# Performance work log

Measured on AMD Instinct MI355X. Metric: run time of the kernel, lower is better.

Reference implementation:

```python
import jax, jax.numpy as jnp
import numpy as np

INPUT, HIDDEN, OUTPUT = 512, 512, 512
B, S = 32, 2048


def setup_inputs() -> dict:
    key = jax.random.key(0)
    ks = jax.random.split(key, 8)
    s_in = 1.0 / np.sqrt(INPUT)
    s_h = 1.0 / np.sqrt(HIDDEN)
    return {
        "x": jax.random.normal(ks[0], (B, S, INPUT), dtype=jnp.float32),
        "W_xh": jax.random.uniform(ks[1], (HIDDEN, INPUT), jnp.float32, -s_in, s_in),
        "b_xh": jax.random.uniform(ks[2], (HIDDEN,), jnp.float32, -s_in, s_in),
        "W_hh": jax.random.uniform(ks[3], (HIDDEN, HIDDEN), jnp.float32, -s_h, s_h),
        "b_hh": jax.random.uniform(ks[4], (HIDDEN,), jnp.float32, -s_h, s_h),
        "b_h": jnp.zeros((HIDDEN,), jnp.float32),
        "W_fc": jax.random.uniform(ks[5], (OUTPUT, HIDDEN), jnp.float32, -s_h, s_h),
        "b_fc": jax.random.uniform(ks[6], (OUTPUT,), jnp.float32, -s_h, s_h),
    }


def reference(x, W_xh, b_xh, W_hh, b_hh, b_h, W_fc, b_fc):
    # Precompute the input projection for all timesteps in one big GEMM:
    # [B,S,I] @ [I,H] -> [B,S,H]; bias terms folded in once.
    xproj = jnp.einsum("bsi,hi->bsh", x, W_xh) + (b_xh + b_hh + b_h)
    h0 = jnp.zeros((x.shape[0], W_hh.shape[0]), x.dtype)

    def step(h, xp_t):
        h = jnp.tanh(xp_t + h @ W_hh.T)
        return h, None

    # scan over time: xproj transposed to [S,B,H]
    h_final, _ = jax.lax.scan(step, h0, jnp.swapaxes(xproj, 0, 1))
    return h_final @ W_fc.T + b_fc
```

## Files before the change

kernel.cpp:

```cpp
#include <hip/hip_runtime.h>

typedef _Float16 f16;
typedef _Float16 f16x8 __attribute__((ext_vector_type(8)));
typedef float    f32x4 __attribute__((ext_vector_type(4)));

#define NSTEP 2048
#define HID   512
#define BATCH 32
#define SEQL  2048

#define P1_AS 40

__global__ __launch_bounds__(256, 2) void xproj_kernel(
    const float* __restrict__ x, const float* __restrict__ Wxh,
    const float* __restrict__ bxh, const float* __restrict__ bhh,
    const float* __restrict__ bh, f16* __restrict__ xp)
{
    __shared__ __align__(16) f16 As[64 * P1_AS];
    __shared__ __align__(16) f16 Bs[512 * P1_AS];

    const int t = threadIdx.x;
    const int wave = t >> 6, lane = t & 63;
    const size_t mbase = (size_t)blockIdx.x * 64;

    f32x4 acc[4][8];
#pragma unroll
    for (int i = 0; i < 4; i++)
#pragma unroll
        for (int j = 0; j < 8; j++) acc[i][j] = (f32x4){0.f, 0.f, 0.f, 0.f};

    const int r_st = t >> 2;
    const int koff = (t & 3) * 8;

    for (int k0 = 0; k0 < 512; k0 += 32) {
        __syncthreads();
        {
            const float* src = x + (mbase + r_st) * 512 + k0 + koff;
            float4 a0 = *(const float4*)src;
            float4 a1 = *(const float4*)(src + 4);
            f16x8 h;
            h[0] = (f16)a0.x; h[1] = (f16)a0.y; h[2] = (f16)a0.z; h[3] = (f16)a0.w;
            h[4] = (f16)a1.x; h[5] = (f16)a1.y; h[6] = (f16)a1.z; h[7] = (f16)a1.w;
            *(f16x8*)&As[r_st * P1_AS + koff] = h;
        }
#pragma unroll
        for (int i = 0; i < 8; i++) {
            int n = r_st + i * 64;
            const float* src = Wxh + (size_t)n * 512 + k0 + koff;
            float4 b0 = *(const float4*)src;
            float4 b1 = *(const float4*)(src + 4);
            f16x8 h;
            h[0] = (f16)b0.x; h[1] = (f16)b0.y; h[2] = (f16)b0.z; h[3] = (f16)b0.w;
            h[4] = (f16)b1.x; h[5] = (f16)b1.y; h[6] = (f16)b1.z; h[7] = (f16)b1.w;
            *(f16x8*)&Bs[n * P1_AS + koff] = h;
        }
        __syncthreads();

        f16x8 af[4];
#pragma unroll
        for (int rt = 0; rt < 4; rt++)
            af[rt] = *(const f16x8*)&As[(rt * 16 + (lane & 15)) * P1_AS + (lane >> 4) * 8];
#pragma unroll
        for (int ct = 0; ct < 8; ct++) {
            f16x8 bf = *(const f16x8*)&Bs[((wave * 8 + ct) * 16 + (lane & 15)) * P1_AS + (lane >> 4) * 8];
#pragma unroll
            for (int rt = 0; rt < 4; rt++)
                acc[rt][ct] = __builtin_amdgcn_mfma_f32_16x16x32_f16(af[rt], bf, acc[rt][ct], 0, 0, 0);
        }
    }

#pragma unroll
    for (int ct = 0; ct < 8; ct++) {
        int n = wave * 128 + ct * 16 + (lane & 15);
        float bias = bxh[n] + bhh[n] + bh[n];
#pragma unroll
        for (int rt = 0; rt < 4; rt++) {
#pragma unroll
            for (int r = 0; r < 4; r++) {
                size_t m = mbase + rt * 16 + (lane >> 4) * 4 + r;
                xp[m * 512 + n] = (f16)(acc[rt][ct][r] + bias);
            }
        }
    }
}

#define P2_LDS_BYTES (2 * HID * 2 + 8 * 16 * 64 * 16)

__global__ __launch_bounds__(512, 2) void rnn_kernel(
    const float* __restrict__ Whh, const f16* __restrict__ xp,
    f16* __restrict__ hfin)
{
    extern __shared__ __align__(16) char smem[];
    f16* hbuf0 = (f16*)smem;
    f16* hbuf1 = hbuf0 + HID;
    f16* ldsB  = hbuf1 + HID;

    const int t = threadIdx.x;
    const int wave = t >> 6, lane = t & 63;
    const int b = blockIdx.x;

    const int c_in = lane & 15;
    const int k8   = (lane >> 4) * 8;

    f16x8 wreg[48];
#pragma unroll
    for (int r = 0; r < 3; r++) {
        const float* wrow = Whh + (size_t)((wave * 4 + r) * 16 + c_in) * 512;
#pragma unroll
        for (int kf = 0; kf < 16; kf++) {
            float4 w0 = *(const float4*)(wrow + kf * 32 + k8);
            float4 w1 = *(const float4*)(wrow + kf * 32 + k8 + 4);
            f16x8 h;
            h[0] = (f16)w0.x; h[1] = (f16)w0.y; h[2] = (f16)w0.z; h[3] = (f16)w0.w;
            h[4] = (f16)w1.x; h[5] = (f16)w1.y; h[6] = (f16)w1.z; h[7] = (f16)w1.w;
            wreg[r * 16 + kf] = h;
        }
    }
    {
        const float* wrow = Whh + (size_t)((wave * 4 + 3) * 16 + c_in) * 512;
#pragma unroll
        for (int kf = 0; kf < 16; kf++) {
            float4 w0 = *(const float4*)(wrow + kf * 32 + k8);
            float4 w1 = *(const float4*)(wrow + kf * 32 + k8 + 4);
            f16x8 h;
            h[0] = (f16)w0.x; h[1] = (f16)w0.y; h[2] = (f16)w0.z; h[3] = (f16)w0.w;
            h[4] = (f16)w1.x; h[5] = (f16)w1.y; h[6] = (f16)w1.z; h[7] = (f16)w1.w;
            *(f16x8*)&ldsB[(size_t)wave * 8192 + kf * 512 + lane * 8] = h;
        }
    }
    hbuf0[t & (HID - 1)] = (f16)0.f;
    __syncthreads();

    const f16* xprow = xp + (size_t)b * SEQL * 512 + wave * 64 + lane;
    const int ldsb_base = wave * 8192 + lane * 8;

    float xv = (float)xprow[0];
    for (int s = 0; s < NSTEP; s++) {
        const f16* cur = (s & 1) ? hbuf1 : hbuf0;
        f16*       nxt = (s & 1) ? hbuf0 : hbuf1;
        int sn = (s + 1 < NSTEP) ? s + 1 : s;
        float xv_next = (float)xprow[(size_t)sn * 512];

        f32x4 a0 = (f32x4){0.f,0.f,0.f,0.f}, a1 = a0, a2 = a0, a3 = a0;
#pragma unroll
        for (int kf = 0; kf < 16; kf++) {
            f16x8 av = *(const f16x8*)&cur[kf * 32 + k8];
            a0 = __builtin_amdgcn_mfma_f32_16x16x32_f16(av, wreg[kf],      a0, 0, 0, 0);
            a1 = __builtin_amdgcn_mfma_f32_16x16x32_f16(av, wreg[16 + kf], a1, 0, 0, 0);
            a2 = __builtin_amdgcn_mfma_f32_16x16x32_f16(av, wreg[32 + kf], a2, 0, 0, 0);
            f16x8 bl = *(const f16x8*)&ldsB[ldsb_base + kf * 512];
            a3 = __builtin_amdgcn_mfma_f32_16x16x32_f16(av, bl, a3, 0, 0, 0);
        }
        int r = lane >> 4;
        float v = (r == 0) ? a0[0] : (r == 1) ? a1[0] : (r == 2) ? a2[0] : a3[0];
        v += xv;
        float e = __expf(2.f * v);
        v = 1.f - 2.f / (e + 1.f);
        nxt[wave * 64 + lane] = (f16)v;
        xv = xv_next;
        __syncthreads();
    }
    hfin[(size_t)b * 512 + t] = hbuf0[t & (HID - 1)];
}

#define P3_HS 520

__global__ __launch_bounds__(256, 2) void fc_kernel(
    const f16* __restrict__ hfin, const float* __restrict__ Wfc,
    const float* __restrict__ bfc, float* __restrict__ out)
{
    __shared__ __align__(16) f16 hs[BATCH * P3_HS];
    const int t = threadIdx.x;
    for (int i = 0; i < 64; i++) {
        int e = i * 256 + t;
        hs[(e >> 9) * P3_HS + (e & 511)] = hfin[e];
    }
    __syncthreads();

    const int bidx = t & 31;
    const int oi = t >> 5;
    const int o0 = blockIdx.x * 16;
    const int oA = o0 + oi, oB = o0 + oi + 8;
    const float* wA = Wfc + (size_t)oA * 512;
    const float* wB = Wfc + (size_t)oB * 512;

    float sA = 0.f, sB = 0.f;
#pragma unroll 4
    for (int kb = 0; kb < 64; kb++) {
        f16x8 hv = *(const f16x8*)&hs[bidx * P3_HS + kb * 8];
        float4 wa0 = *(const float4*)(wA + kb * 8);
        float4 wa1 = *(const float4*)(wA + kb * 8 + 4);
        float4 wb0 = *(const float4*)(wB + kb * 8);
        float4 wb1 = *(const float4*)(wB + kb * 8 + 4);
        float h0 = (float)hv[0], h1 = (float)hv[1], h2 = (float)hv[2], h3 = (float)hv[3];
        float h4 = (float)hv[4], h5 = (float)hv[5], h6 = (float)hv[6], h7 = (float)hv[7];
        sA += wa0.x*h0 + wa0.y*h1 + wa0.z*h2 + wa0.w*h3 + wa1.x*h4 + wa1.y*h5 + wa1.z*h6 + wa1.w*h7;
        sB += wb0.x*h0 + wb0.y*h1 + wb0.z*h2 + wb0.w*h3 + wb1.x*h4 + wb1.y*h5 + wb1.z*h6 + wb1.w*h7;
    }
    out[(size_t)bidx * 512 + oA] = sA + bfc[oA];
    out[(size_t)bidx * 512 + oB] = sB + bfc[oB];
}

extern "C" void kernel_launch(void* const* d_in, const int* in_sizes, int n_in,
                              void* d_out, int out_size, void* d_ws, size_t ws_size,
                              hipStream_t stream) {
    const float* x    = (const float*)d_in[0];
    const float* Wxh  = (const float*)d_in[1];
    const float* bxh  = (const float*)d_in[2];
    const float* Whh  = (const float*)d_in[3];
    const float* bhh  = (const float*)d_in[4];
    const float* bh   = (const float*)d_in[5];
    const float* Wfc  = (const float*)d_in[6];
    const float* bfc  = (const float*)d_in[7];
    float* outp = (float*)d_out;

    f16* xp   = (f16*)d_ws;
    f16* hfin = (f16*)((char*)d_ws + (size_t)BATCH * SEQL * 512 * 2);

    hipFuncSetAttribute((const void*)rnn_kernel,
                        hipFuncAttributeMaxDynamicSharedMemorySize, 160 * 1024);

    xproj_kernel<<<(BATCH * SEQL) / 64, 256, 0, stream>>>(x, Wxh, bxh, bhh, bh, xp);
    rnn_kernel<<<BATCH, 512, P2_LDS_BYTES, stream>>>(Whh, xp, hfin);
    fc_kernel<<<32, 256, 0, stream>>>(hfin, Wfc, bfc, outp);
}
```

Before: 2.796 ms.

## Split recurrent matvec between MFMA and packed fdot2 with all weights in registers

The recurrent step now gives each wave 16 hidden outputs computed by one MFMA chain, plus 48 outputs computed with packed f16 dot-product instructions. All of W_hh is held in registers, which removes the per-step LDS weight reads and the dynamic shared memory. The old version ran four MFMAs per k-slice and used only one row of each result, so most MFMA work was wasted. The cost is extra VALU dot instructions, cross-lane shuffle reductions, four tanh evaluations per lane, and much higher register pressure, with launch bounds dropped to one block per CU.

```diff
diff --git a/kernel.cpp b/kernel.cpp
--- a/kernel.cpp
+++ b/kernel.cpp
@@ -1,6 +1,7 @@
 #include <hip/hip_runtime.h>
 
 typedef _Float16 f16;
+typedef _Float16 f16x2 __attribute__((ext_vector_type(2)));
 typedef _Float16 f16x8 __attribute__((ext_vector_type(8)));
 typedef float    f32x4 __attribute__((ext_vector_type(4)));
 
@@ -8,6 +9,14 @@
 #define HID   512
 #define BATCH 32
 #define SEQL  2048
+
+#if __has_builtin(__builtin_amdgcn_fdot2)
+#define FDOT2(a, b, c) __builtin_amdgcn_fdot2((a), (b), (c), false)
+#else
+static __device__ __forceinline__ float FDOT2(f16x2 a, f16x2 b, float c) {
+    return c + (float)a[0] * (float)b[0] + (float)a[1] * (float)b[1];
+}
+#endif
 
 #define P1_AS 40
 
@@ -84,28 +93,23 @@
     }
 }
 
-#define P2_LDS_BYTES (2 * HID * 2 + 8 * 16 * 64 * 16)
-
-__global__ __launch_bounds__(512, 2) void rnn_kernel(
+__global__ __launch_bounds__(512, 1) void rnn_kernel(
     const float* __restrict__ Whh, const f16* __restrict__ xp,
     f16* __restrict__ hfin)
 {
-    extern __shared__ __align__(16) char smem[];
-    f16* hbuf0 = (f16*)smem;
-    f16* hbuf1 = hbuf0 + HID;
-    f16* ldsB  = hbuf1 + HID;
+    __shared__ __align__(16) f16 hbuf[2][HID];
 
     const int t = threadIdx.x;
     const int wave = t >> 6, lane = t & 63;
     const int b = blockIdx.x;
 
     const int c_in = lane & 15;
-    const int k8   = (lane >> 4) * 8;
-
-    f16x8 wreg[48];
-#pragma unroll
-    for (int r = 0; r < 3; r++) {
-        const float* wrow = Whh + (size_t)((wave * 4 + r) * 16 + c_in) * 512;
+    const int q    = lane >> 4;
+    const int k8   = q * 8;
+
+    f16x8 wreg[16];
+    {
+        const float* wrow = Whh + (size_t)(wave * 16 + c_in) * 512;
 #pragma unroll
         for (int kf = 0; kf < 16; kf++) {
             float4 w0 = *(const float4*)(wrow + kf * 32 + k8);
@@ -113,54 +117,90 @@
             f16x8 h;
             h[0] = (f16)w0.x; h[1] = (f16)w0.y; h[2] = (f16)w0.z; h[3] = (f16)w0.w;
             h[4] = (f16)w1.x; h[5] = (f16)w1.y; h[6] = (f16)w1.z; h[7] = (f16)w1.w;
-            wreg[r * 16 + kf] = h;
-        }
-    }
-    {
-        const float* wrow = Whh + (size_t)((wave * 4 + 3) * 16 + c_in) * 512;
-#pragma unroll
-        for (int kf = 0; kf < 16; kf++) {
-            float4 w0 = *(const float4*)(wrow + kf * 32 + k8);
-            float4 w1 = *(const float4*)(wrow + kf * 32 + k8 + 4);
-            f16x8 h;
-            h[0] = (f16)w0.x; h[1] = (f16)w0.y; h[2] = (f16)w0.z; h[3] = (f16)w0.w;
-            h[4] = (f16)w1.x; h[5] = (f16)w1.y; h[6] = (f16)w1.z; h[7] = (f16)w1.w;
-            *(f16x8*)&ldsB[(size_t)wave * 8192 + kf * 512 + lane * 8] = h;
-        }
-    }
-    hbuf0[t & (HID - 1)] = (f16)0.f;
+            wreg[kf] = h;
+        }
+    }
+    const int nv0 = 128 + wave * 48 + c_in;
+    const int nv1 = nv0 + 16;
+    const int nv2 = nv0 + 32;
+    f16x8 w0r[16], w1r[16], w2r[16];
+#pragma unroll
+    for (int kf = 0; kf < 16; kf++) {
+        const float* p0 = Whh + (size_t)nv0 * 512 + kf * 32 + k8;
+        const float* p1 = Whh + (size_t)nv1 * 512 + kf * 32 + k8;
+        const float* p2 = Whh + (size_t)nv2 * 512 + kf * 32 + k8;
+        float4 a0 = *(const float4*)p0, a1 = *(const float4*)(p0 + 4);
+        float4 b0 = *(const float4*)p1, b1 = *(const float4*)(p1 + 4);
+        float4 c0 = *(const float4*)p2, c1 = *(const float4*)(p2 + 4);
+        f16x8 ha, hb, hc;
+        ha[0]=(f16)a0.x; ha[1]=(f16)a0.y; ha[2]=(f16)a0.z; ha[3]=(f16)a0.w;
+        ha[4]=(f16)a1.x; ha[5]=(f16)a1.y; ha[6]=(f16)a1.z; ha[7]=(f16)a1.w;
+        hb[0]=(f16)b0.x; hb[1]=(f16)b0.y; hb[2]=(f16)b0.z; hb[3]=(f16)b0.w;
+        hb[4]=(f16)b1.x; hb[5]=(f16)b1.y; hb[6]=(f16)b1.z; hb[7]=(f16)b1.w;
+        hc[0]=(f16)c0.x; hc[1]=(f16)c0.y; hc[2]=(f16)c0.z; hc[3]=(f16)c0.w;
+        hc[4]=(f16)c1.x; hc[5]=(f16)c1.y; hc[6]=(f16)c1.z; hc[7]=(f16)c1.w;
+        w0r[kf] = ha; w1r[kf] = hb; w2r[kf] = hc;
+    }
+
+    hbuf[0][t & (HID - 1)] = (f16)0.f;
     __syncthreads();
 
-    const f16* xprow = xp + (size_t)b * SEQL * 512 + wave * 64 + lane;
-    const int ldsb_base = wave * 8192 + lane * 8;
-
-    float xv = (float)xprow[0];
+    const size_t xbase = (size_t)b * SEQL * 512;
+    const int nm = wave * 16 + c_in;
+
+    float xm = (float)xp[xbase + nm];
+    float x0 = (float)xp[xbase + nv0];
+    float x1 = (float)xp[xbase + nv1];
+    float x2 = (float)xp[xbase + nv2];
+
     for (int s = 0; s < NSTEP; s++) {
-        const f16* cur = (s & 1) ? hbuf1 : hbuf0;
-        f16*       nxt = (s & 1) ? hbuf0 : hbuf1;
-        int sn = (s + 1 < NSTEP) ? s + 1 : s;
-        float xv_next = (float)xprow[(size_t)sn * 512];
-
-        f32x4 a0 = (f32x4){0.f,0.f,0.f,0.f}, a1 = a0, a2 = a0, a3 = a0;
+        const f16* cur = hbuf[s & 1];
+        f16*       nxt = hbuf[(s & 1) ^ 1];
+        size_t nb = xbase + (size_t)((s + 1 < NSTEP) ? s + 1 : s) * 512;
+        float xmn = (float)xp[nb + nm];
+        float x0n = (float)xp[nb + nv0];
+        float x1n = (float)xp[nb + nv1];
+        float x2n = (float)xp[nb + nv2];
+
+        f32x4 acc = (f32x4){0.f, 0.f, 0.f, 0.f};
+        float s0 = 0.f, s1 = 0.f, s2 = 0.f;
 #pragma unroll
         for (int kf = 0; kf < 16; kf++) {
             f16x8 av = *(const f16x8*)&cur[kf * 32 + k8];
-            a0 = __builtin_amdgcn_mfma_f32_16x16x32_f16(av, wreg[kf],      a0, 0, 0, 0);
-            a1 = __builtin_amdgcn_mfma_f32_16x16x32_f16(av, wreg[16 + kf], a1, 0, 0, 0);
-            a2 = __builtin_amdgcn_mfma_f32_16x16x32_f16(av, wreg[32 + kf], a2, 0, 0, 0);
-            f16x8 bl = *(const f16x8*)&ldsB[ldsb_base + kf * 512];
-            a3 = __builtin_amdgcn_mfma_f32_16x16x32_f16(av, bl, a3, 0, 0, 0);
-        }
-        int r = lane >> 4;
-        float v = (r == 0) ? a0[0] : (r == 1) ? a1[0] : (r == 2) ? a2[0] : a3[0];
-        v += xv;
-        float e = __expf(2.f * v);
-        v = 1.f - 2.f / (e + 1.f);
-        nxt[wave * 64 + lane] = (f16)v;
-        xv = xv_next;
+            acc = __builtin_amdgcn_mfma_f32_16x16x32_f16(av, wreg[kf], acc, 0, 0, 0);
+            f16x8 wa = w0r[kf], wb = w1r[kf], wc = w2r[kf];
+#define RNN_DOT3(P)                                                            \
+            do {                                                               \
+                f16x2 hp = __builtin_shufflevector(av, av, 2*(P), 2*(P)+1);    \
+                s0 = FDOT2(hp, __builtin_shufflevector(wa, wa, 2*(P), 2*(P)+1), s0); \
+                s1 = FDOT2(hp, __builtin_shufflevector(wb, wb, 2*(P), 2*(P)+1), s1); \
+                s2 = FDOT2(hp, __builtin_shufflevector(wc, wc, 2*(P), 2*(P)+1), s2); \
+            } while (0)
+            RNN_DOT3(0); RNN_DOT3(1); RNN_DOT3(2); RNN_DOT3(3);
+#undef RNN_DOT3
+        }
+        s0 += __shfl_xor(s0, 16, 64); s0 += __shfl_xor(s0, 32, 64);
+        s1 += __shfl_xor(s1, 16, 64); s1 += __shfl_xor(s1, 32, 64);
+        s2 += __shfl_xor(s2, 16, 64); s2 += __shfl_xor(s2, 32, 64);
+
+        if (q == 0) {
+            float vm = acc[0] + xm;
+            float v0 = s0 + x0;
+            float v1 = s1 + x1;
+            float v2 = s2 + x2;
+            vm = 1.f - 2.f / (__expf(2.f * vm) + 1.f);
+            v0 = 1.f - 2.f / (__expf(2.f * v0) + 1.f);
+            v1 = 1.f - 2.f / (__expf(2.f * v1) + 1.f);
+            v2 = 1.f - 2.f / (__expf(2.f * v2) + 1.f);
+            nxt[nm]  = (f16)vm;
+            nxt[nv0] = (f16)v0;
+            nxt[nv1] = (f16)v1;
+            nxt[nv2] = (f16)v2;
+        }
+        xm = xmn; x0 = x0n; x1 = x1n; x2 = x2n;
         __syncthreads();
     }
-    hfin[(size_t)b * 512 + t] = hbuf0[t & (HID - 1)];
+    hfin[(size_t)b * 512 + t] = hbuf[0][t & (HID - 1)];
 }
 
 #define P3_HS 520
@@ -217,10 +257,7 @@
     f16* xp   = (f16*)d_ws;
     f16* hfin = (f16*)((char*)d_ws + (size_t)BATCH * SEQL * 512 * 2);
 
-    hipFuncSetAttribute((const void*)rnn_kernel,
-                        hipFuncAttributeMaxDynamicSharedMemorySize, 160 * 1024);
-
     xproj_kernel<<<(BATCH * SEQL) / 64, 256, 0, stream>>>(x, Wxh, bxh, bhh, bh, xp);
-    rnn_kernel<<<BATCH, 512, P2_LDS_BYTES, stream>>>(Whh, xp, hfin);
+    rnn_kernel<<<BATCH, 512, 0, stream>>>(Whh, xp, hfin);
     fc_kernel<<<32, 256, 0, stream>>>(hfin, Wfc, bfc, outp);
 }
```

After: 5.837 ms. 109% more time.

## Replace half of recurrent MFMAs with packed fp16 dot products plus lane reductions

Applied to the files above, without the earlier changes.

In the sequential RNN step, each wave now computes two of its four 16-column tiles with MFMA and the other two with v_dot2 fp16 dot products spread across the four lane groups, finished by cross-lane xor shuffles. This targets MFMA latency on the serial per-step critical path, where only one useful row of each MFMA output is consumed. The cost is extra VALU dot instructions and shuffles per step, and output columns are remapped so each wave owns a contiguous 32 columns plus two 16-column strips in the upper half.

```diff
diff --git a/kernel.cpp b/kernel.cpp
--- a/kernel.cpp
+++ b/kernel.cpp
@@ -1,6 +1,7 @@
 #include <hip/hip_runtime.h>
 
 typedef _Float16 f16;
+typedef _Float16 f16x2 __attribute__((ext_vector_type(2)));
 typedef _Float16 f16x8 __attribute__((ext_vector_type(8)));
 typedef float    f32x4 __attribute__((ext_vector_type(4)));
 
@@ -8,6 +9,26 @@
 #define HID   512
 #define BATCH 32
 #define SEQL  2048
+
+#if __has_builtin(__builtin_amdgcn_fdot2)
+#define FDOT2(a, b, c) __builtin_amdgcn_fdot2((a), (b), (c), false)
+#else
+static __device__ __forceinline__ float FDOT2(f16x2 a, f16x2 b, float c) {
+    return c + (float)a[0] * (float)b[0] + (float)a[1] * (float)b[1];
+}
+#endif
+
+#define RNN_DOT8(AV, W, S)                                                  \
+    do {                                                                    \
+        S = FDOT2(__builtin_shufflevector(AV, AV, 0, 1),                    \
+                  __builtin_shufflevector(W, W, 0, 1), S);                  \
+        S = FDOT2(__builtin_shufflevector(AV, AV, 2, 3),                    \
+                  __builtin_shufflevector(W, W, 2, 3), S);                  \
+        S = FDOT2(__builtin_shufflevector(AV, AV, 4, 5),                    \
+                  __builtin_shufflevector(W, W, 4, 5), S);                  \
+        S = FDOT2(__builtin_shufflevector(AV, AV, 6, 7),                    \
+                  __builtin_shufflevector(W, W, 6, 7), S);                  \
+    } while (0)
 
 #define P1_AS 40
 
@@ -84,7 +105,7 @@
     }
 }
 
-#define P2_LDS_BYTES (2 * HID * 2 + 8 * 16 * 64 * 16)
+#define P2_LDS_BYTES (2 * HID * 2 + 8 * 16 * 4 * 16 * 8 * 2)
 
 __global__ __launch_bounds__(512, 2) void rnn_kernel(
     const float* __restrict__ Whh, const f16* __restrict__ xp,
@@ -93,19 +114,20 @@
     extern __shared__ __align__(16) char smem[];
     f16* hbuf0 = (f16*)smem;
     f16* hbuf1 = hbuf0 + HID;
-    f16* ldsB  = hbuf1 + HID;
+    f16* wlds  = hbuf1 + HID;
 
     const int t = threadIdx.x;
     const int wave = t >> 6, lane = t & 63;
     const int b = blockIdx.x;
 
     const int c_in = lane & 15;
-    const int k8   = (lane >> 4) * 8;
-
-    f16x8 wreg[48];
-#pragma unroll
-    for (int r = 0; r < 3; r++) {
-        const float* wrow = Whh + (size_t)((wave * 4 + r) * 16 + c_in) * 512;
+    const int q    = lane >> 4;
+    const int k8   = q * 8;
+
+    f16x8 wreg[32];
+#pragma unroll
+    for (int tt = 0; tt < 2; tt++) {
+        const float* wrow = Whh + (size_t)(wave * 32 + tt * 16 + c_in) * 512;
 #pragma unroll
         for (int kf = 0; kf < 16; kf++) {
             float4 w0 = *(const float4*)(wrow + kf * 32 + k8);
@@ -113,11 +135,24 @@
             f16x8 h;
             h[0] = (f16)w0.x; h[1] = (f16)w0.y; h[2] = (f16)w0.z; h[3] = (f16)w0.w;
             h[4] = (f16)w1.x; h[5] = (f16)w1.y; h[6] = (f16)w1.z; h[7] = (f16)w1.w;
-            wreg[r * 16 + kf] = h;
-        }
-    }
+            wreg[tt * 16 + kf] = h;
+        }
+    }
+    const int nr = 256 + wave * 16 + c_in;
+    f16x8 wv[16];
+#pragma unroll
+    for (int kf = 0; kf < 16; kf++) {
+        const float* p = Whh + (size_t)nr * 512 + kf * 32 + k8;
+        float4 w0 = *(const float4*)p;
+        float4 w1 = *(const float4*)(p + 4);
+        f16x8 h;
+        h[0] = (f16)w0.x; h[1] = (f16)w0.y; h[2] = (f16)w0.z; h[3] = (f16)w0.w;
+        h[4] = (f16)w1.x; h[5] = (f16)w1.y; h[6] = (f16)w1.z; h[7] = (f16)w1.w;
+        wv[kf] = h;
+    }
+    const int nl = 384 + wave * 16 + c_in;
     {
-        const float* wrow = Whh + (size_t)((wave * 4 + 3) * 16 + c_in) * 512;
+        const float* wrow = Whh + (size_t)nl * 512;
 #pragma unroll
         for (int kf = 0; kf < 16; kf++) {
             float4 w0 = *(const float4*)(wrow + kf * 32 + k8);
@@ -125,38 +160,45 @@
             f16x8 h;
             h[0] = (f16)w0.x; h[1] = (f16)w0.y; h[2] = (f16)w0.z; h[3] = (f16)w0.w;
             h[4] = (f16)w1.x; h[5] = (f16)w1.y; h[6] = (f16)w1.z; h[7] = (f16)w1.w;
-            *(f16x8*)&ldsB[(size_t)wave * 8192 + kf * 512 + lane * 8] = h;
-        }
-    }
+            *(f16x8*)&wlds[wave * 8192 + kf * 512 + (q * 16 + c_in) * 8] = h;
+        }
+    }
+
     hbuf0[t & (HID - 1)] = (f16)0.f;
     __syncthreads();
 
-    const f16* xprow = xp + (size_t)b * SEQL * 512 + wave * 64 + lane;
-    const int ldsb_base = wave * 8192 + lane * 8;
-
-    float xv = (float)xprow[0];
+    const int out_col = (q == 0) ? (wave * 32 + c_in)
+                      : (q == 1) ? (wave * 32 + 16 + c_in)
+                      : (q == 2) ? nr : nl;
+    const size_t xbase = (size_t)b * SEQL * 512;
+    const int wbase = wave * 8192 + (q * 16 + c_in) * 8;
+
+    float xv = (float)xp[xbase + out_col];
     for (int s = 0; s < NSTEP; s++) {
         const f16* cur = (s & 1) ? hbuf1 : hbuf0;
         f16*       nxt = (s & 1) ? hbuf0 : hbuf1;
         int sn = (s + 1 < NSTEP) ? s + 1 : s;
-        float xv_next = (float)xprow[(size_t)sn * 512];
-
-        f32x4 a0 = (f32x4){0.f,0.f,0.f,0.f}, a1 = a0, a2 = a0, a3 = a0;
+        float xv_next = (float)xp[xbase + (size_t)sn * 512 + out_col];
+
+        f32x4 acc0 = (f32x4){0.f, 0.f, 0.f, 0.f}, acc1 = acc0;
+        float sr = 0.f, sl = 0.f;
 #pragma unroll
         for (int kf = 0; kf < 16; kf++) {
             f16x8 av = *(const f16x8*)&cur[kf * 32 + k8];
-            a0 = __builtin_amdgcn_mfma_f32_16x16x32_f16(av, wreg[kf],      a0, 0, 0, 0);
-            a1 = __builtin_amdgcn_mfma_f32_16x16x32_f16(av, wreg[16 + kf], a1, 0, 0, 0);
-            a2 = __builtin_amdgcn_mfma_f32_16x16x32_f16(av, wreg[32 + kf], a2, 0, 0, 0);
-            f16x8 bl = *(const f16x8*)&ldsB[ldsb_base + kf * 512];
-            a3 = __builtin_amdgcn_mfma_f32_16x16x32_f16(av, bl, a3, 0, 0, 0);
-        }
-        int r = lane >> 4;
-        float v = (r == 0) ? a0[0] : (r == 1) ? a1[0] : (r == 2) ? a2[0] : a3[0];
+            f16x8 bl = *(const f16x8*)&wlds[wbase + kf * 512];
+            acc0 = __builtin_amdgcn_mfma_f32_16x16x32_f16(av, wreg[kf],      acc0, 0, 0, 0);
+            acc1 = __builtin_amdgcn_mfma_f32_16x16x32_f16(av, wreg[16 + kf], acc1, 0, 0, 0);
+            RNN_DOT8(av, wv[kf], sr);
+            RNN_DOT8(av, bl, sl);
+        }
+        sr += __shfl_xor(sr, 16, 64); sr += __shfl_xor(sr, 32, 64);
+        sl += __shfl_xor(sl, 16, 64); sl += __shfl_xor(sl, 32, 64);
+
+        float v = (q == 0) ? acc0[0] : (q == 1) ? acc1[0] : (q == 2) ? sr : sl;
         v += xv;
         float e = __expf(2.f * v);
         v = 1.f - 2.f / (e + 1.f);
-        nxt[wave * 64 + lane] = (f16)v;
+        nxt[out_col] = (f16)v;
         xv = xv_next;
         __syncthreads();
     }
```

Result: slower. 3.575 ms (+27.9%).
